# Optimization experiments

Measured on AMD Instinct MI355X. Metric: run time of the kernel, lower is better.

## Reference

```python
import jax, jax.numpy as jnp
import numpy as np

B, S, D, H = 4, 2048, 1024, 16
HD = D // H

def setup_inputs() -> dict:
    key = jax.random.key(0)
    ks = jax.random.split(key, 9)
    s = 1.0 / np.sqrt(D)
    return {
        "x": jax.random.normal(ks[0], (B, S, D), dtype=jnp.float32),
        "wq": jax.random.uniform(ks[1], (D, D), jnp.float32, -s, s),
        "bq": jnp.zeros((D,), jnp.float32),
        "wk": jax.random.uniform(ks[2], (D, D), jnp.float32, -s, s),
        "bk": jnp.zeros((D,), jnp.float32),
        "wv": jax.random.uniform(ks[3], (D, D), jnp.float32, -s, s),
        "bv": jnp.zeros((D,), jnp.float32),
        "wo": jax.random.uniform(ks[4], (D, D), jnp.float32, -s, s),
        "bo": jnp.zeros((D,), jnp.float32),
    }

def reference(x, wq, bq, wk, bk, wv, bv, wo, bo):
    b, s, _ = x.shape
    # project and split heads: [B,S,D] -> [B,H,S,HD]
    def heads(w, bias):
        return (x @ w.T + bias).reshape(b, s, H, HD).transpose(0, 2, 1, 3)
    q = heads(wq, bq)
    k = heads(wk, bk)
    v = heads(wv, bv)
    scale = 1.0 / jnp.sqrt(jnp.float32(HD))
    scores = jnp.einsum("bhqd,bhkd->bhqk", q, k) * scale
    attn = jax.nn.softmax(scores, axis=-1)
    out = jnp.einsum("bhqk,bhkd->bhqd", attn, v)
    out = out.transpose(0, 2, 1, 3).reshape(b, s, D)
    return out @ wo.T + bo
```

## Files before the change

### kernel.cpp

```cpp
#include <hip/hip_runtime.h>
#include <stdint.h>


#define B_ 4
#define S_ 2048
#define D_ 1024
#define H_ 16
#define HD_ 64
#define M_ (B_ * S_)

typedef __bf16 bf16x8 __attribute__((ext_vector_type(8)));
typedef float f32x4 __attribute__((ext_vector_type(4)));
typedef float f32x16 __attribute__((ext_vector_type(16)));
typedef unsigned short u16;

#define QSCALE 0.18033688011112042f
#define THR2 11.0f

__device__ __forceinline__ u16 f2bf(float f) {
  union { float f; unsigned u; } v; v.f = f;
  unsigned u = v.u;
  u += 0x7fff + ((u >> 16) & 1);
  return (u16)(u >> 16);
}

__device__ __forceinline__ float exp2_fast(float x) {
#if __has_builtin(__builtin_amdgcn_exp2f)
  return __builtin_amdgcn_exp2f(x);
#else
  return __expf(x * 0.69314718056f);
#endif
}

__device__ __forceinline__ unsigned packbf(float a, float b) {
  union { unsigned u; __bf16 h[2]; } v;
  v.h[0] = (__bf16)a; v.h[1] = (__bf16)b;
  return v.u;
}

__device__ __forceinline__ void gl2lds16(const void* g, void* l) {
  __builtin_amdgcn_global_load_lds(
      (const __attribute__((address_space(1))) unsigned int*)g,
      (__attribute__((address_space(3))) unsigned int*)l, 16, 0, 0);
}

__global__ __launch_bounds__(256) void convert_kernel(
    const float* __restrict__ x, const float* __restrict__ wq,
    const float* __restrict__ wk, const float* __restrict__ wv,
    const float* __restrict__ wo, u16* __restrict__ xb, u16* __restrict__ wqb,
    u16* __restrict__ wkb, u16* __restrict__ wvb, u16* __restrict__ wob) {
  const int64_t NX = (int64_t)M_ * D_ / 4;
  const int64_t NW = (int64_t)D_ * D_ / 4;
  int64_t i = (int64_t)blockIdx.x * blockDim.x + threadIdx.x;
  const float* src; u16* dst; int64_t off;
  if (i < NX)              { src = x;  dst = xb;  off = i; }
  else if (i < NX + NW)    { src = wq; dst = wqb; off = i - NX; }
  else if (i < NX + 2*NW)  { src = wk; dst = wkb; off = i - NX - NW; }
  else if (i < NX + 3*NW)  { src = wv; dst = wvb; off = i - NX - 2*NW; }
  else                     { src = wo; dst = wob; off = i - NX - 3*NW; }
  float4 v = reinterpret_cast<const float4*>(src)[off];
  ushort4 o;
  o.x = f2bf(v.x); o.y = f2bf(v.y); o.z = f2bf(v.z); o.w = f2bf(v.w);
  reinterpret_cast<ushort4*>(dst)[off] = o;
}

template <int MODE>
__global__ __launch_bounds__(256) void gemm_kernel(
    const u16* __restrict__ A, const u16* __restrict__ Bw,
    const float* __restrict__ bias, void* __restrict__ out) {
  __shared__ u16 As[128 * 64];
  __shared__ u16 Bs[128 * 64];
  const int tid = threadIdx.x;
  const int lane = tid & 63;
  const int wid = tid >> 6;
  const int row0 = blockIdx.y * 128;
  const int col0 = blockIdx.x * 128;
  const int wr = (wid >> 1) * 64;
  const int wc = (wid & 1) * 64;

  f32x4 acc[4][4] = {};
  const int srow = lane >> 3;
  const int cc = (lane & 7) ^ srow;

  for (int kt = 0; kt < D_; kt += 64) {
    __syncthreads();
    for (int t = 0; t < 4; ++t) {
      int r = (wid * 4 + t) * 8 + srow;
      gl2lds16(A + (int64_t)(row0 + r) * D_ + kt + cc * 8,
               (char*)As + (wid * 4 + t) * 1024);
      gl2lds16(Bw + (int64_t)(col0 + r) * D_ + kt + cc * 8,
               (char*)Bs + (wid * 4 + t) * 1024);
    }
    __syncthreads();

    bf16x8 af[4][2], bfr[4][2];
#pragma unroll
    for (int mi = 0; mi < 4; ++mi)
#pragma unroll
      for (int ks = 0; ks < 2; ++ks) {
        int c = ks * 4 + (lane >> 4);
        int ra = wr + mi * 16 + (lane & 15);
        af[mi][ks] = *reinterpret_cast<const bf16x8*>(
            (char*)As + ra * 128 + ((c ^ (ra & 7)) << 4));
        int rb = wc + mi * 16 + (lane & 15);
        bfr[mi][ks] = *reinterpret_cast<const bf16x8*>(
            (char*)Bs + rb * 128 + ((c ^ (rb & 7)) << 4));
      }
#pragma unroll
    for (int ks = 0; ks < 2; ++ks)
#pragma unroll
      for (int mi = 0; mi < 4; ++mi)
#pragma unroll
        for (int ni = 0; ni < 4; ++ni) {
          if (MODE == 1)
            acc[mi][ni] = __builtin_amdgcn_mfma_f32_16x16x32_bf16(
                bfr[ni][ks], af[mi][ks], acc[mi][ni], 0, 0, 0);
          else
            acc[mi][ni] = __builtin_amdgcn_mfma_f32_16x16x32_bf16(
                af[mi][ks], bfr[ni][ks], acc[mi][ni], 0, 0, 0);
        }
  }

  if (MODE == 0 || MODE == 3) {
    u16* o = (u16*)out;
#pragma unroll
    for (int mi = 0; mi < 4; ++mi)
#pragma unroll
      for (int ni = 0; ni < 4; ++ni) {
        int j = col0 + wc + ni * 16 + (lane & 15);
        float bvv = bias[j];
        int h = j >> 6, hd = j & 63;
#pragma unroll
        for (int r = 0; r < 4; ++r) {
          int i = row0 + wr + mi * 16 + (lane >> 4) * 4 + r;
          int b = i >> 11, s = i & 2047;
          float val = acc[mi][ni][r] + bvv;
          if (MODE == 3) val *= QSCALE;
          o[((int64_t)(b * H_ + h) * S_ + s) * HD_ + hd] = f2bf(val);
        }
      }
  } else if (MODE == 1) {
    u16* o = (u16*)out;
#pragma unroll
    for (int mi = 0; mi < 4; ++mi)
#pragma unroll
      for (int ni = 0; ni < 4; ++ni) {
        int i = row0 + wr + mi * 16 + (lane & 15);
        int b = i >> 11, s = i & 2047;
#pragma unroll
        for (int r = 0; r < 4; ++r) {
          int j = col0 + wc + ni * 16 + (lane >> 4) * 4 + r;
          int h = j >> 6, hd = j & 63;
          o[((int64_t)(b * H_ + h) * HD_ + hd) * S_ + s] = f2bf(acc[mi][ni][r] + bias[j]);
        }
      }
  } else {
    float* o = (float*)out;
#pragma unroll
    for (int mi = 0; mi < 4; ++mi)
#pragma unroll
      for (int ni = 0; ni < 4; ++ni) {
        int j = col0 + wc + ni * 16 + (lane & 15);
        float bvv = bias[j];
#pragma unroll
        for (int r = 0; r < 4; ++r) {
          int i = row0 + wr + mi * 16 + (lane >> 4) * 4 + r;
          o[(int64_t)i * D_ + j] = acc[mi][ni][r] + bvv;
        }
      }
  }
}

__global__ __launch_bounds__(256) void attn_kernel(
    const u16* __restrict__ Q, const u16* __restrict__ Kg,
    const u16* __restrict__ Vt, u16* __restrict__ AO) {
  __shared__ u16 Ks[2][64 * 64];
  __shared__ u16 Vs[2][64 * 64];
  const int tid = threadIdx.x;
  const int lane = tid & 63;
  const int l31 = lane & 31;
  const int hi = lane >> 5;
  const int wid = tid >> 6;
  const int orig = blockIdx.x;
  const int swz = (orig & 7) * 128 + (orig >> 3);
  const int bh = swz >> 4;
  const int qw = (swz & 15) * 128 + wid * 32;

  bf16x8 qf[4];
#pragma unroll
  for (int ks = 0; ks < 4; ++ks)
    qf[ks] = *reinterpret_cast<const bf16x8*>(
        Q + ((int64_t)bh * S_ + qw + l31) * HD_ + ks * 16 + hi * 8);

  f32x16 o0 = {}, o1 = {};
  float mrow = -1e30f, lrow = 0.f;

  const int srow = lane >> 3;
  const int cc = (lane & 7) ^ srow;

#pragma unroll
  for (int tt = 0; tt < 2; ++tt) {
    int r = (wid * 2 + tt) * 8 + srow;
    gl2lds16(Kg + ((int64_t)bh * S_ + r) * HD_ + cc * 8,
             (char*)Ks[0] + (wid * 2 + tt) * 1024);
    gl2lds16(Vt + ((int64_t)bh * HD_ + r) * S_ + cc * 8,
             (char*)Vs[0] + (wid * 2 + tt) * 1024);
  }

  const int NT = S_ / 64;
  for (int t = 0; t < NT; ++t) {
    const int cur = t & 1;
    asm volatile("s_waitcnt vmcnt(0)" ::: "memory");
    __builtin_amdgcn_s_barrier();
    if (t + 1 < NT) {
      int kv0 = (t + 1) * 64;
#pragma unroll
      for (int tt = 0; tt < 2; ++tt) {
        int r = (wid * 2 + tt) * 8 + srow;
        gl2lds16(Kg + ((int64_t)bh * S_ + kv0 + r) * HD_ + cc * 8,
                 (char*)Ks[cur ^ 1] + (wid * 2 + tt) * 1024);
        gl2lds16(Vt + ((int64_t)bh * HD_ + r) * S_ + kv0 + cc * 8,
                 (char*)Vs[cur ^ 1] + (wid * 2 + tt) * 1024);
      }
    }

    f32x16 sc0 = {}, sc1 = {};
    {
      const char* kbase = (const char*)Ks[cur];
      __builtin_amdgcn_s_setprio(1);
#pragma unroll
      for (int ks = 0; ks < 4; ++ks) {
        int chunk = 2 * ks + hi;
        int r0 = l31, r1 = 32 + l31;
        bf16x8 k0 = *reinterpret_cast<const bf16x8*>(
            kbase + r0 * 128 + ((chunk ^ (r0 & 7)) << 4));
        bf16x8 k1 = *reinterpret_cast<const bf16x8*>(
            kbase + r1 * 128 + ((chunk ^ (r1 & 7)) << 4));
        sc0 = __builtin_amdgcn_mfma_f32_32x32x16_bf16(k0, qf[ks], sc0, 0, 0, 0);
        sc1 = __builtin_amdgcn_mfma_f32_32x32x16_bf16(k1, qf[ks], sc1, 0, 0, 0);
      }
      __builtin_amdgcn_s_setprio(0);
    }

    float a8[8];
#pragma unroll
    for (int i = 0; i < 8; ++i)
      a8[i] = fmaxf(fmaxf(sc0[2 * i], sc0[2 * i + 1]),
                    fmaxf(sc1[2 * i], sc1[2 * i + 1]));
    float mx = fmaxf(fmaxf(fmaxf(a8[0], a8[1]), fmaxf(a8[2], a8[3])),
                     fmaxf(fmaxf(a8[4], a8[5]), fmaxf(a8[6], a8[7])));
    mx = fmaxf(mx, __shfl_xor(mx, 32));
    if (!__all((mx - mrow <= THR2) ? 1 : 0)) {
      float mnew = fmaxf(mrow, mx);
      float al = exp2_fast(mrow - mnew);
      mrow = mnew;
      lrow *= al;
#pragma unroll
      for (int tt = 0; tt < 16; ++tt) {
        float at = __shfl(al, (tt & 3) + 8 * (tt >> 2) + 4 * hi);
        o0[tt] *= at; o1[tt] *= at;
      }
    }
#pragma unroll
    for (int tt = 0; tt < 16; ++tt) {
      sc0[tt] = exp2_fast(sc0[tt] - mrow);
      sc1[tt] = exp2_fast(sc1[tt] - mrow);
    }
    float s8[8];
#pragma unroll
    for (int i = 0; i < 8; ++i)
      s8[i] = (sc0[2 * i] + sc0[2 * i + 1]) + (sc1[2 * i] + sc1[2 * i + 1]);
    float rs = ((s8[0] + s8[1]) + (s8[2] + s8[3])) +
               ((s8[4] + s8[5]) + (s8[6] + s8[7]));
    rs += __shfl_xor(rs, 32);
    lrow += rs;

    unsigned w0[4][2], w1[4][2];
#pragma unroll
    for (int rr = 0; rr < 4; ++rr)
#pragma unroll
      for (int h2 = 0; h2 < 2; ++h2) {
        w0[rr][h2] = packbf(sc0[4 * rr + 2 * h2], sc0[4 * rr + 2 * h2 + 1]);
        w1[rr][h2] = packbf(sc1[4 * rr + 2 * h2], sc1[4 * rr + 2 * h2 + 1]);
      }
    unsigned rv0[2][2], rv1[2][2];
#pragma unroll
    for (int c = 0; c < 2; ++c)
#pragma unroll
      for (int h2 = 0; h2 < 2; ++h2) {
        rv0[c][h2] = (unsigned)__shfl_xor(
            (int)(hi ? w0[2 * c][h2] : w0[2 * c + 1][h2]), 32);
        rv1[c][h2] = (unsigned)__shfl_xor(
            (int)(hi ? w1[2 * c][h2] : w1[2 * c + 1][h2]), 32);
      }

    {
      const char* vbase = (const char*)Vs[cur];
      __builtin_amdgcn_s_setprio(1);
#pragma unroll
      for (int kb = 0; kb < 4; ++kb) {
        const int c = kb & 1;
        union { bf16x8 v; unsigned u[4]; } pu;
        if (kb < 2) {
          pu.u[0] = hi ? rv0[c][0] : w0[2 * c][0];
          pu.u[1] = hi ? rv0[c][1] : w0[2 * c][1];
          pu.u[2] = hi ? w0[2 * c + 1][0] : rv0[c][0];
          pu.u[3] = hi ? w0[2 * c + 1][1] : rv0[c][1];
        } else {
          pu.u[0] = hi ? rv1[c][0] : w1[2 * c][0];
          pu.u[1] = hi ? rv1[c][1] : w1[2 * c][1];
          pu.u[2] = hi ? w1[2 * c + 1][0] : rv1[c][0];
          pu.u[3] = hi ? w1[2 * c + 1][1] : rv1[c][1];
        }
        int chunk = 2 * kb + hi;
        int r0 = l31, r1 = 32 + l31;
        bf16x8 v0 = *reinterpret_cast<const bf16x8*>(
            vbase + r0 * 128 + ((chunk ^ (r0 & 7)) << 4));
        bf16x8 v1 = *reinterpret_cast<const bf16x8*>(
            vbase + r1 * 128 + ((chunk ^ (r1 & 7)) << 4));
        o0 = __builtin_amdgcn_mfma_f32_32x32x16_bf16(pu.v, v0, o0, 0, 0, 0);
        o1 = __builtin_amdgcn_mfma_f32_32x32x16_bf16(pu.v, v1, o1, 0, 0, 0);
      }
      __builtin_amdgcn_s_setprio(0);
    }
  }

  const int b = bh >> 4, h = bh & 15;
  float linv = __builtin_amdgcn_rcpf(lrow);
#pragma unroll
  for (int tt = 0; tt < 16; ++tt) {
    int row = (tt & 3) + 8 * (tt >> 2) + 4 * hi;
    float inv = __shfl(linv, row);
    int qr = qw + row;
    int64_t base = ((int64_t)(b * S_ + qr)) * D_ + h * HD_ + l31;
    AO[base] = f2bf(o0[tt] * inv);
    AO[base + 32] = f2bf(o1[tt] * inv);
  }
}

extern "C" void kernel_launch(void* const* d_in, const int* in_sizes, int n_in,
                              void* d_out, int out_size, void* d_ws, size_t ws_size,
                              hipStream_t stream) {
  const float* x  = (const float*)d_in[0];
  const float* wq = (const float*)d_in[1];
  const float* bq = (const float*)d_in[2];
  const float* wk = (const float*)d_in[3];
  const float* bk = (const float*)d_in[4];
  const float* wv = (const float*)d_in[5];
  const float* bv = (const float*)d_in[6];
  const float* wo = (const float*)d_in[7];
  const float* bo = (const float*)d_in[8];
  char* ws = (char*)d_ws;
  u16* xb  = (u16*)ws;
  u16* wqb = (u16*)(ws + (16ll << 20));
  u16* wkb = (u16*)(ws + (18ll << 20));
  u16* wvb = (u16*)(ws + (20ll << 20));
  u16* wob = (u16*)(ws + (22ll << 20));
  u16* q   = (u16*)(ws + (24ll << 20));
  u16* k   = (u16*)(ws + (40ll << 20));
  u16* vt  = (u16*)(ws + (56ll << 20));
  u16* ao  = xb;

  convert_kernel<<<12288, 256, 0, stream>>>(x, wq, wk, wv, wo, xb, wqb, wkb, wvb, wob);
  dim3 gg(D_ / 128, M_ / 128);
  gemm_kernel<3><<<gg, 256, 0, stream>>>(xb, wqb, bq, q);
  gemm_kernel<0><<<gg, 256, 0, stream>>>(xb, wkb, bk, k);
  gemm_kernel<1><<<gg, 256, 0, stream>>>(xb, wvb, bv, vt);
  attn_kernel<<<1024, 256, 0, stream>>>(q, k, vt, ao);
  gemm_kernel<2><<<gg, 256, 0, stream>>>(ao, wob, bo, (float*)d_out);
}
```

Baseline: 249.5 us.

## Fuse QKV projections into one launch and defer softmax cross-lane reductions

Merges the three separate Q/K/V projection GEMM launches into a single grid of 24x64 blocks, with each block choosing its weight, bias and output layout from blockIdx.x. This removes two kernel launches and their tail effects and lets one larger grid fill the GPU. In the attention kernel, the cross-half-wave max shuffle now runs only inside the rare rescale branch, and the row-sum shuffle runs once after the loop instead of every tile. The trade-off is per-block branching on the weight index in the fused GEMM, and the skip test now uses each half-wave's own partial max.

```diff
diff --git a/kernel.cpp b/kernel.cpp
--- a/kernel.cpp
+++ b/kernel.cpp
@@ -64,17 +64,22 @@
   reinterpret_cast<ushort4*>(dst)[off] = o;
 }
 
-template <int MODE>
-__global__ __launch_bounds__(256) void gemm_kernel(
-    const u16* __restrict__ A, const u16* __restrict__ Bw,
-    const float* __restrict__ bias, void* __restrict__ out) {
+__global__ __launch_bounds__(256) void gemm_qkv_kernel(
+    const u16* __restrict__ A, const u16* __restrict__ wqb,
+    const u16* __restrict__ wkb, const u16* __restrict__ wvb,
+    const float* __restrict__ bq, const float* __restrict__ bk,
+    const float* __restrict__ bv, u16* __restrict__ oq, u16* __restrict__ ok,
+    u16* __restrict__ ovt) {
   __shared__ u16 As[128 * 64];
   __shared__ u16 Bs[128 * 64];
+  const int widx = blockIdx.x >> 3;
+  const int col0 = (blockIdx.x & 7) * 128;
+  const int row0 = blockIdx.y * 128;
+  const u16* Bw = (widx == 0) ? wqb : ((widx == 1) ? wkb : wvb);
+  const float* bias = (widx == 0) ? bq : ((widx == 1) ? bk : bv);
   const int tid = threadIdx.x;
   const int lane = tid & 63;
   const int wid = tid >> 6;
-  const int row0 = blockIdx.y * 128;
-  const int col0 = blockIdx.x * 128;
   const int wr = (wid >> 1) * 64;
   const int wc = (wid & 1) * 64;
 
@@ -106,23 +111,30 @@
         bfr[mi][ks] = *reinterpret_cast<const bf16x8*>(
             (char*)Bs + rb * 128 + ((c ^ (rb & 7)) << 4));
       }
-#pragma unroll
-    for (int ks = 0; ks < 2; ++ks)
-#pragma unroll
-      for (int mi = 0; mi < 4; ++mi)
-#pragma unroll
-        for (int ni = 0; ni < 4; ++ni) {
-          if (MODE == 1)
+    if (widx == 2) {
+#pragma unroll
+      for (int ks = 0; ks < 2; ++ks)
+#pragma unroll
+        for (int mi = 0; mi < 4; ++mi)
+#pragma unroll
+          for (int ni = 0; ni < 4; ++ni)
             acc[mi][ni] = __builtin_amdgcn_mfma_f32_16x16x32_bf16(
                 bfr[ni][ks], af[mi][ks], acc[mi][ni], 0, 0, 0);
-          else
+    } else {
+#pragma unroll
+      for (int ks = 0; ks < 2; ++ks)
+#pragma unroll
+        for (int mi = 0; mi < 4; ++mi)
+#pragma unroll
+          for (int ni = 0; ni < 4; ++ni)
             acc[mi][ni] = __builtin_amdgcn_mfma_f32_16x16x32_bf16(
                 af[mi][ks], bfr[ni][ks], acc[mi][ni], 0, 0, 0);
-        }
-  }
-
-  if (MODE == 0 || MODE == 3) {
-    u16* o = (u16*)out;
+    }
+  }
+
+  if (widx != 2) {
+    u16* o = (widx == 0) ? oq : ok;
+    const float sc = (widx == 0) ? QSCALE : 1.0f;
 #pragma unroll
     for (int mi = 0; mi < 4; ++mi)
 #pragma unroll
@@ -134,13 +146,11 @@
         for (int r = 0; r < 4; ++r) {
           int i = row0 + wr + mi * 16 + (lane >> 4) * 4 + r;
           int b = i >> 11, s = i & 2047;
-          float val = acc[mi][ni][r] + bvv;
-          if (MODE == 3) val *= QSCALE;
-          o[((int64_t)(b * H_ + h) * S_ + s) * HD_ + hd] = f2bf(val);
+          o[((int64_t)(b * H_ + h) * S_ + s) * HD_ + hd] =
+              f2bf((acc[mi][ni][r] + bvv) * sc);
         }
       }
-  } else if (MODE == 1) {
-    u16* o = (u16*)out;
+  } else {
 #pragma unroll
     for (int mi = 0; mi < 4; ++mi)
 #pragma unroll
@@ -151,24 +161,76 @@
         for (int r = 0; r < 4; ++r) {
           int j = col0 + wc + ni * 16 + (lane >> 4) * 4 + r;
           int h = j >> 6, hd = j & 63;
-          o[((int64_t)(b * H_ + h) * HD_ + hd) * S_ + s] = f2bf(acc[mi][ni][r] + bias[j]);
+          ovt[((int64_t)(b * H_ + h) * HD_ + hd) * S_ + s] =
+              f2bf(acc[mi][ni][r] + bias[j]);
         }
       }
-  } else {
-    float* o = (float*)out;
+  }
+}
+
+__global__ __launch_bounds__(256) void gemm_out_kernel(
+    const u16* __restrict__ A, const u16* __restrict__ Bw,
+    const float* __restrict__ bias, float* __restrict__ out) {
+  __shared__ u16 As[128 * 64];
+  __shared__ u16 Bs[128 * 64];
+  const int row0 = blockIdx.y * 128;
+  const int col0 = blockIdx.x * 128;
+  const int tid = threadIdx.x;
+  const int lane = tid & 63;
+  const int wid = tid >> 6;
+  const int wr = (wid >> 1) * 64;
+  const int wc = (wid & 1) * 64;
+
+  f32x4 acc[4][4] = {};
+  const int srow = lane >> 3;
+  const int cc = (lane & 7) ^ srow;
+
+  for (int kt = 0; kt < D_; kt += 64) {
+    __syncthreads();
+    for (int t = 0; t < 4; ++t) {
+      int r = (wid * 4 + t) * 8 + srow;
+      gl2lds16(A + (int64_t)(row0 + r) * D_ + kt + cc * 8,
+               (char*)As + (wid * 4 + t) * 1024);
+      gl2lds16(Bw + (int64_t)(col0 + r) * D_ + kt + cc * 8,
+               (char*)Bs + (wid * 4 + t) * 1024);
+    }
+    __syncthreads();
+
+    bf16x8 af[4][2], bfr[4][2];
 #pragma unroll
     for (int mi = 0; mi < 4; ++mi)
 #pragma unroll
-      for (int ni = 0; ni < 4; ++ni) {
-        int j = col0 + wc + ni * 16 + (lane & 15);
-        float bvv = bias[j];
-#pragma unroll
-        for (int r = 0; r < 4; ++r) {
-          int i = row0 + wr + mi * 16 + (lane >> 4) * 4 + r;
-          o[(int64_t)i * D_ + j] = acc[mi][ni][r] + bvv;
-        }
-      }
-  }
+      for (int ks = 0; ks < 2; ++ks) {
+        int c = ks * 4 + (lane >> 4);
+        int ra = wr + mi * 16 + (lane & 15);
+        af[mi][ks] = *reinterpret_cast<const bf16x8*>(
+            (char*)As + ra * 128 + ((c ^ (ra & 7)) << 4));
+        int rb = wc + mi * 16 + (lane & 15);
+        bfr[mi][ks] = *reinterpret_cast<const bf16x8*>(
+            (char*)Bs + rb * 128 + ((c ^ (rb & 7)) << 4));
+      }
+#pragma unroll
+    for (int ks = 0; ks < 2; ++ks)
+#pragma unroll
+      for (int mi = 0; mi < 4; ++mi)
+#pragma unroll
+        for (int ni = 0; ni < 4; ++ni)
+          acc[mi][ni] = __builtin_amdgcn_mfma_f32_16x16x32_bf16(
+              af[mi][ks], bfr[ni][ks], acc[mi][ni], 0, 0, 0);
+  }
+
+#pragma unroll
+  for (int mi = 0; mi < 4; ++mi)
+#pragma unroll
+    for (int ni = 0; ni < 4; ++ni) {
+      int j = col0 + wc + ni * 16 + (lane & 15);
+      float bvv = bias[j];
+#pragma unroll
+      for (int r = 0; r < 4; ++r) {
+        int i = row0 + wr + mi * 16 + (lane >> 4) * 4 + r;
+        out[(int64_t)i * D_ + j] = acc[mi][ni][r] + bvv;
+      }
+    }
 }
 
 __global__ __launch_bounds__(256) void attn_kernel(
@@ -193,7 +255,8 @@
         Q + ((int64_t)bh * S_ + qw + l31) * HD_ + ks * 16 + hi * 8);
 
   f32x16 o0 = {}, o1 = {};
-  float mrow = -1e30f, lrow = 0.f;
+  float mrow = -1e30f;
+  float lrow = 0.f;
 
   const int srow = lane >> 3;
   const int cc = (lane & 7) ^ srow;
@@ -245,13 +308,13 @@
     float a8[8];
 #pragma unroll
     for (int i = 0; i < 8; ++i)
-      a8[i] = fmaxf(fmaxf(sc0[2 * i], sc0[2 * i + 1]),
-                    fmaxf(sc1[2 * i], sc1[2 * i + 1]));
-    float mx = fmaxf(fmaxf(fmaxf(a8[0], a8[1]), fmaxf(a8[2], a8[3])),
-                     fmaxf(fmaxf(a8[4], a8[5]), fmaxf(a8[6], a8[7])));
-    mx = fmaxf(mx, __shfl_xor(mx, 32));
+      a8[i] = fmaxf(fmaxf(fmaxf(sc0[2 * i], sc0[2 * i + 1]), sc1[2 * i]),
+                    sc1[2 * i + 1]);
+    float mx = fmaxf(fmaxf(fmaxf(fmaxf(a8[0], a8[1]), a8[2]), a8[3]),
+                     fmaxf(fmaxf(fmaxf(a8[4], a8[5]), a8[6]), a8[7]));
     if (!__all((mx - mrow <= THR2) ? 1 : 0)) {
-      float mnew = fmaxf(mrow, mx);
+      float mxf = fmaxf(mx, __shfl_xor(mx, 32));
+      float mnew = fmaxf(mrow, mxf);
       float al = exp2_fast(mrow - mnew);
       mrow = mnew;
       lrow *= al;
@@ -270,10 +333,8 @@
 #pragma unroll
     for (int i = 0; i < 8; ++i)
       s8[i] = (sc0[2 * i] + sc0[2 * i + 1]) + (sc1[2 * i] + sc1[2 * i + 1]);
-    float rs = ((s8[0] + s8[1]) + (s8[2] + s8[3])) +
-               ((s8[4] + s8[5]) + (s8[6] + s8[7]));
-    rs += __shfl_xor(rs, 32);
-    lrow += rs;
+    lrow += ((s8[0] + s8[1]) + (s8[2] + s8[3])) +
+            ((s8[4] + s8[5]) + (s8[6] + s8[7]));
 
     unsigned w0[4][2], w1[4][2];
 #pragma unroll
@@ -325,6 +386,7 @@
     }
   }
 
+  lrow += __shfl_xor(lrow, 32);
   const int b = bh >> 4, h = bh & 15;
   float linv = __builtin_amdgcn_rcpf(lrow);
 #pragma unroll
@@ -362,10 +424,8 @@
   u16* ao  = xb;
 
   convert_kernel<<<12288, 256, 0, stream>>>(x, wq, wk, wv, wo, xb, wqb, wkb, wvb, wob);
-  dim3 gg(D_ / 128, M_ / 128);
-  gemm_kernel<3><<<gg, 256, 0, stream>>>(xb, wqb, bq, q);
-  gemm_kernel<0><<<gg, 256, 0, stream>>>(xb, wkb, bk, k);
-  gemm_kernel<1><<<gg, 256, 0, stream>>>(xb, wvb, bv, vt);
+  gemm_qkv_kernel<<<dim3(24, 64), 256, 0, stream>>>(xb, wqb, wkb, wvb, bq, bk, bv,
+                                                    q, k, vt);
   attn_kernel<<<1024, 256, 0, stream>>>(q, k, vt, ao);
-  gemm_kernel<2><<<gg, 256, 0, stream>>>(ao, wob, bo, (float*)d_out);
-}
+  gemm_out_kernel<<<dim3(8, 64), 256, 0, stream>>>(ao, wob, bo, (float*)d_out);
+}
```

New measurement: 285.5 us. +14.4%, slower.

## Compute softmax row sums via MFMA with ones and unroll KV loop by two

Applied to the files above, without the earlier changes.

Replaces the per-tile VALU reduction of exp scores and the cross-lane shuffle with an extra MFMA against a ones vector, so row sums accumulate in a matrix accumulator already laid out to match the output. It also unrolls the KV loop by two using a macro so buffer indices become compile-time constants, and it uses incrementing pointers for the K/V prefetch. The max shuffle now runs only on the rescale path. The cost is one extra MFMA per kb step (a 50% increase in PV MFMAs) and 16 more accumulator registers, which could hurt occupancy. Row sums are now built from bf16-rounded probabilities, which slightly changes numerics.

```diff
diff --git a/kernel.cpp b/kernel.cpp
--- a/kernel.cpp
+++ b/kernel.cpp
@@ -192,145 +192,141 @@
     qf[ks] = *reinterpret_cast<const bf16x8*>(
         Q + ((int64_t)bh * S_ + qw + l31) * HD_ + ks * 16 + hi * 8);
 
-  f32x16 o0 = {}, o1 = {};
-  float mrow = -1e30f, lrow = 0.f;
+  bf16x8 ones8;
+#pragma unroll
+  for (int i = 0; i < 8; ++i) ones8[i] = (__bf16)1.0f;
+
+  f32x16 o0 = {}, o1 = {}, ls = {};
+  float mrow = -1e30f;
 
   const int srow = lane >> 3;
   const int cc = (lane & 7) ^ srow;
 
-#pragma unroll
-  for (int tt = 0; tt < 2; ++tt) {
-    int r = (wid * 2 + tt) * 8 + srow;
-    gl2lds16(Kg + ((int64_t)bh * S_ + r) * HD_ + cc * 8,
-             (char*)Ks[0] + (wid * 2 + tt) * 1024);
-    gl2lds16(Vt + ((int64_t)bh * HD_ + r) * S_ + cc * 8,
-             (char*)Vs[0] + (wid * 2 + tt) * 1024);
-  }
+  const u16* kp0 = Kg + ((int64_t)bh * S_ + (wid * 2 + 0) * 8 + srow) * HD_ + cc * 8;
+  const u16* kp1 = Kg + ((int64_t)bh * S_ + (wid * 2 + 1) * 8 + srow) * HD_ + cc * 8;
+  const u16* vp0 = Vt + ((int64_t)bh * HD_ + (wid * 2 + 0) * 8 + srow) * S_ + cc * 8;
+  const u16* vp1 = Vt + ((int64_t)bh * HD_ + (wid * 2 + 1) * 8 + srow) * S_ + cc * 8;
+
+  gl2lds16(kp0, (char*)Ks[0] + (wid * 2 + 0) * 1024); kp0 += 64 * HD_;
+  gl2lds16(kp1, (char*)Ks[0] + (wid * 2 + 1) * 1024); kp1 += 64 * HD_;
+  gl2lds16(vp0, (char*)Vs[0] + (wid * 2 + 0) * 1024); vp0 += 64;
+  gl2lds16(vp1, (char*)Vs[0] + (wid * 2 + 1) * 1024); vp1 += 64;
 
   const int NT = S_ / 64;
-  for (int t = 0; t < NT; ++t) {
-    const int cur = t & 1;
-    asm volatile("s_waitcnt vmcnt(0)" ::: "memory");
-    __builtin_amdgcn_s_barrier();
-    if (t + 1 < NT) {
-      int kv0 = (t + 1) * 64;
-#pragma unroll
-      for (int tt = 0; tt < 2; ++tt) {
-        int r = (wid * 2 + tt) * 8 + srow;
-        gl2lds16(Kg + ((int64_t)bh * S_ + kv0 + r) * HD_ + cc * 8,
-                 (char*)Ks[cur ^ 1] + (wid * 2 + tt) * 1024);
-        gl2lds16(Vt + ((int64_t)bh * HD_ + r) * S_ + kv0 + cc * 8,
-                 (char*)Vs[cur ^ 1] + (wid * 2 + tt) * 1024);
-      }
-    }
-
-    f32x16 sc0 = {}, sc1 = {};
-    {
-      const char* kbase = (const char*)Ks[cur];
-      __builtin_amdgcn_s_setprio(1);
-#pragma unroll
-      for (int ks = 0; ks < 4; ++ks) {
-        int chunk = 2 * ks + hi;
-        int r0 = l31, r1 = 32 + l31;
-        bf16x8 k0 = *reinterpret_cast<const bf16x8*>(
-            kbase + r0 * 128 + ((chunk ^ (r0 & 7)) << 4));
-        bf16x8 k1 = *reinterpret_cast<const bf16x8*>(
-            kbase + r1 * 128 + ((chunk ^ (r1 & 7)) << 4));
-        sc0 = __builtin_amdgcn_mfma_f32_32x32x16_bf16(k0, qf[ks], sc0, 0, 0, 0);
-        sc1 = __builtin_amdgcn_mfma_f32_32x32x16_bf16(k1, qf[ks], sc1, 0, 0, 0);
-      }
-      __builtin_amdgcn_s_setprio(0);
-    }
-
-    float a8[8];
-#pragma unroll
-    for (int i = 0; i < 8; ++i)
-      a8[i] = fmaxf(fmaxf(sc0[2 * i], sc0[2 * i + 1]),
-                    fmaxf(sc1[2 * i], sc1[2 * i + 1]));
-    float mx = fmaxf(fmaxf(fmaxf(a8[0], a8[1]), fmaxf(a8[2], a8[3])),
-                     fmaxf(fmaxf(a8[4], a8[5]), fmaxf(a8[6], a8[7])));
-    mx = fmaxf(mx, __shfl_xor(mx, 32));
-    if (!__all((mx - mrow <= THR2) ? 1 : 0)) {
-      float mnew = fmaxf(mrow, mx);
-      float al = exp2_fast(mrow - mnew);
-      mrow = mnew;
-      lrow *= al;
-#pragma unroll
-      for (int tt = 0; tt < 16; ++tt) {
-        float at = __shfl(al, (tt & 3) + 8 * (tt >> 2) + 4 * hi);
-        o0[tt] *= at; o1[tt] *= at;
-      }
-    }
-#pragma unroll
-    for (int tt = 0; tt < 16; ++tt) {
-      sc0[tt] = exp2_fast(sc0[tt] - mrow);
-      sc1[tt] = exp2_fast(sc1[tt] - mrow);
-    }
-    float s8[8];
-#pragma unroll
-    for (int i = 0; i < 8; ++i)
-      s8[i] = (sc0[2 * i] + sc0[2 * i + 1]) + (sc1[2 * i] + sc1[2 * i + 1]);
-    float rs = ((s8[0] + s8[1]) + (s8[2] + s8[3])) +
-               ((s8[4] + s8[5]) + (s8[6] + s8[7]));
-    rs += __shfl_xor(rs, 32);
-    lrow += rs;
-
-    unsigned w0[4][2], w1[4][2];
-#pragma unroll
-    for (int rr = 0; rr < 4; ++rr)
-#pragma unroll
-      for (int h2 = 0; h2 < 2; ++h2) {
-        w0[rr][h2] = packbf(sc0[4 * rr + 2 * h2], sc0[4 * rr + 2 * h2 + 1]);
-        w1[rr][h2] = packbf(sc1[4 * rr + 2 * h2], sc1[4 * rr + 2 * h2 + 1]);
-      }
-    unsigned rv0[2][2], rv1[2][2];
-#pragma unroll
-    for (int c = 0; c < 2; ++c)
-#pragma unroll
-      for (int h2 = 0; h2 < 2; ++h2) {
-        rv0[c][h2] = (unsigned)__shfl_xor(
-            (int)(hi ? w0[2 * c][h2] : w0[2 * c + 1][h2]), 32);
-        rv1[c][h2] = (unsigned)__shfl_xor(
-            (int)(hi ? w1[2 * c][h2] : w1[2 * c + 1][h2]), 32);
-      }
-
-    {
-      const char* vbase = (const char*)Vs[cur];
-      __builtin_amdgcn_s_setprio(1);
-#pragma unroll
-      for (int kb = 0; kb < 4; ++kb) {
-        const int c = kb & 1;
-        union { bf16x8 v; unsigned u[4]; } pu;
-        if (kb < 2) {
-          pu.u[0] = hi ? rv0[c][0] : w0[2 * c][0];
-          pu.u[1] = hi ? rv0[c][1] : w0[2 * c][1];
-          pu.u[2] = hi ? w0[2 * c + 1][0] : rv0[c][0];
-          pu.u[3] = hi ? w0[2 * c + 1][1] : rv0[c][1];
-        } else {
-          pu.u[0] = hi ? rv1[c][0] : w1[2 * c][0];
-          pu.u[1] = hi ? rv1[c][1] : w1[2 * c][1];
-          pu.u[2] = hi ? w1[2 * c + 1][0] : rv1[c][0];
-          pu.u[3] = hi ? w1[2 * c + 1][1] : rv1[c][1];
-        }
-        int chunk = 2 * kb + hi;
-        int r0 = l31, r1 = 32 + l31;
-        bf16x8 v0 = *reinterpret_cast<const bf16x8*>(
-            vbase + r0 * 128 + ((chunk ^ (r0 & 7)) << 4));
-        bf16x8 v1 = *reinterpret_cast<const bf16x8*>(
-            vbase + r1 * 128 + ((chunk ^ (r1 & 7)) << 4));
-        o0 = __builtin_amdgcn_mfma_f32_32x32x16_bf16(pu.v, v0, o0, 0, 0, 0);
-        o1 = __builtin_amdgcn_mfma_f32_32x32x16_bf16(pu.v, v1, o1, 0, 0, 0);
-      }
-      __builtin_amdgcn_s_setprio(0);
-    }
-  }
+
+#define TILE_STEP(T, CUR)                                                      \
+  {                                                                            \
+    asm volatile("s_waitcnt vmcnt(0)" ::: "memory");                           \
+    __builtin_amdgcn_s_barrier();                                              \
+    if ((T) + 1 < NT) {                                                        \
+      gl2lds16(kp0, (char*)Ks[(CUR) ^ 1] + (wid * 2 + 0) * 1024);              \
+      gl2lds16(kp1, (char*)Ks[(CUR) ^ 1] + (wid * 2 + 1) * 1024);              \
+      gl2lds16(vp0, (char*)Vs[(CUR) ^ 1] + (wid * 2 + 0) * 1024);              \
+      gl2lds16(vp1, (char*)Vs[(CUR) ^ 1] + (wid * 2 + 1) * 1024);              \
+      kp0 += 64 * HD_; kp1 += 64 * HD_; vp0 += 64; vp1 += 64;                  \
+    }                                                                          \
+    f32x16 sc0 = {}, sc1 = {};                                                 \
+    {                                                                          \
+      const char* kbase = (const char*)Ks[CUR];                                \
+      __builtin_amdgcn_s_setprio(1);                                           \
+      _Pragma("unroll")                                                        \
+      for (int ks = 0; ks < 4; ++ks) {                                         \
+        int chunk = 2 * ks + hi;                                               \
+        int r0 = l31, r1 = 32 + l31;                                           \
+        bf16x8 k0 = *reinterpret_cast<const bf16x8*>(                          \
+            kbase + r0 * 128 + ((chunk ^ (r0 & 7)) << 4));                     \
+        bf16x8 k1 = *reinterpret_cast<const bf16x8*>(                          \
+            kbase + r1 * 128 + ((chunk ^ (r1 & 7)) << 4));                     \
+        sc0 = __builtin_amdgcn_mfma_f32_32x32x16_bf16(k0, qf[ks], sc0, 0, 0, 0); \
+        sc1 = __builtin_amdgcn_mfma_f32_32x32x16_bf16(k1, qf[ks], sc1, 0, 0, 0); \
+      }                                                                        \
+      __builtin_amdgcn_s_setprio(0);                                           \
+    }                                                                          \
+    float a8[8];                                                               \
+    _Pragma("unroll")                                                          \
+    for (int i = 0; i < 8; ++i)                                                \
+      a8[i] = fmaxf(fmaxf(fmaxf(sc0[2 * i], sc0[2 * i + 1]), sc1[2 * i]),      \
+                    sc1[2 * i + 1]);                                           \
+    float mx = fmaxf(fmaxf(fmaxf(fmaxf(a8[0], a8[1]), a8[2]), a8[3]),          \
+                     fmaxf(fmaxf(fmaxf(a8[4], a8[5]), a8[6]), a8[7]));         \
+    if (!__all((mx - mrow <= THR2) ? 1 : 0)) {                                 \
+      float mxf = fmaxf(mx, __shfl_xor(mx, 32));                               \
+      float mnew = fmaxf(mrow, mxf);                                           \
+      float al = exp2_fast(mrow - mnew);                                       \
+      mrow = mnew;                                                             \
+      _Pragma("unroll")                                                        \
+      for (int tt = 0; tt < 16; ++tt) {                                        \
+        float at = __shfl(al, (tt & 3) + 8 * (tt >> 2) + 4 * hi);              \
+        o0[tt] *= at; o1[tt] *= at; ls[tt] *= at;                              \
+      }                                                                        \
+    }                                                                          \
+    _Pragma("unroll")                                                          \
+    for (int tt = 0; tt < 16; ++tt) {                                          \
+      sc0[tt] = exp2_fast(sc0[tt] - mrow);                                     \
+      sc1[tt] = exp2_fast(sc1[tt] - mrow);                                     \
+    }                                                                          \
+    unsigned w0[4][2], w1[4][2];                                               \
+    _Pragma("unroll")                                                          \
+    for (int rr = 0; rr < 4; ++rr) {                                           \
+      w0[rr][0] = packbf(sc0[4 * rr], sc0[4 * rr + 1]);                        \
+      w0[rr][1] = packbf(sc0[4 * rr + 2], sc0[4 * rr + 3]);                    \
+      w1[rr][0] = packbf(sc1[4 * rr], sc1[4 * rr + 1]);                        \
+      w1[rr][1] = packbf(sc1[4 * rr + 2], sc1[4 * rr + 3]);                    \
+    }                                                                          \
+    unsigned rv0[2][2], rv1[2][2];                                             \
+    _Pragma("unroll")                                                          \
+    for (int c = 0; c < 2; ++c) {                                              \
+      _Pragma("unroll")                                                        \
+      for (int h2 = 0; h2 < 2; ++h2) {                                         \
+        rv0[c][h2] = (unsigned)__shfl_xor(                                     \
+            (int)(hi ? w0[2 * c][h2] : w0[2 * c + 1][h2]), 32);                \
+        rv1[c][h2] = (unsigned)__shfl_xor(                                     \
+            (int)(hi ? w1[2 * c][h2] : w1[2 * c + 1][h2]), 32);                \
+      }                                                                        \
+    }                                                                          \
+    {                                                                          \
+      const char* vbase = (const char*)Vs[CUR];                                \
+      __builtin_amdgcn_s_setprio(1);                                           \
+      _Pragma("unroll")                                                        \
+      for (int kb = 0; kb < 4; ++kb) {                                         \
+        const int c = kb & 1;                                                  \
+        union { bf16x8 v; unsigned u[4]; } pu;                                 \
+        if (kb < 2) {                                                          \
+          pu.u[0] = hi ? rv0[c][0] : w0[2 * c][0];                             \
+          pu.u[1] = hi ? rv0[c][1] : w0[2 * c][1];                             \
+          pu.u[2] = hi ? w0[2 * c + 1][0] : rv0[c][0];                         \
+          pu.u[3] = hi ? w0[2 * c + 1][1] : rv0[c][1];                         \
+        } else {                                                               \
+          pu.u[0] = hi ? rv1[c][0] : w1[2 * c][0];                             \
+          pu.u[1] = hi ? rv1[c][1] : w1[2 * c][1];                             \
+          pu.u[2] = hi ? w1[2 * c + 1][0] : rv1[c][0];                         \
+          pu.u[3] = hi ? w1[2 * c + 1][1] : rv1[c][1];                         \
+        }                                                                      \
+        int chunk = 2 * kb + hi;                                               \
+        int r0 = l31, r1 = 32 + l31;                                           \
+        bf16x8 v0 = *reinterpret_cast<const bf16x8*>(                          \
+            vbase + r0 * 128 + ((chunk ^ (r0 & 7)) << 4));                     \
+        bf16x8 v1 = *reinterpret_cast<const bf16x8*>(                          \
+            vbase + r1 * 128 + ((chunk ^ (r1 & 7)) << 4));                     \
+        o0 = __builtin_amdgcn_mfma_f32_32x32x16_bf16(pu.v, v0, o0, 0, 0, 0);   \
+        o1 = __builtin_amdgcn_mfma_f32_32x32x16_bf16(pu.v, v1, o1, 0, 0, 0);   \
+        ls = __builtin_amdgcn_mfma_f32_32x32x16_bf16(pu.v, ones8, ls, 0, 0, 0);\
+      }                                                                        \
+      __builtin_amdgcn_s_setprio(0);                                           \
+    }                                                                          \
+  }
+
+  for (int t = 0; t < NT; t += 2) {
+    TILE_STEP(t, 0)
+    TILE_STEP(t + 1, 1)
+  }
+#undef TILE_STEP
 
   const int b = bh >> 4, h = bh & 15;
-  float linv = __builtin_amdgcn_rcpf(lrow);
 #pragma unroll
   for (int tt = 0; tt < 16; ++tt) {
     int row = (tt & 3) + 8 * (tt >> 2) + 4 * hi;
-    float inv = __shfl(linv, row);
+    float inv = __builtin_amdgcn_rcpf(ls[tt]);
     int qr = qw + row;
     int64_t base = ((int64_t)(b * S_ + qr)) * D_ + h * HD_ + l31;
     AO[base] = f2bf(o0[tt] * inv);
```

After: 249.9 us. About the same (+0.2%).
